# Kernel tuning notes

Hardware: AMD Instinct MI355X
Metric: run time of the kernel (lower is better)

## Reference

```python
import jax, jax.numpy as jnp
import numpy as np
from jax import lax
from jax.scipy.special import logsumexp

KX = jnp.array([[1., 0., -1.], [2., 0., -2.], [1., 0., -1.]], jnp.float32).reshape(1, 1, 3, 3)
KY = jnp.array([[1., 2., 1.], [0., 0., 0.], [-1., -2., -1.]], jnp.float32).reshape(1, 1, 3, 3)
SINK_EPS = 0.05 ** 2  # geomloss SamplesLoss('sinkhorn', p=2, blur=0.05): eps = blur**p
SINK_ITERS = 10
N_SUB = 4096


def _gauss1d(size, sigma):
    x = jnp.arange(size, dtype=jnp.float32) - (size - 1) / 2.0
    k = jnp.exp(-(x * x) / (2.0 * sigma * sigma))
    return k / k.sum()


def _sep_filter(x, k, sym_pad):
    # separable 2D filter; x [B,C,H,W], k [ks]. VALID conv; optional symmetric pad (scipy 'reflect').
    B, C, H, W = x.shape
    xr = x.reshape(B * C, 1, H, W)
    if sym_pad:
        r = k.shape[0] // 2
        xr = jnp.pad(xr, ((0, 0), (0, 0), (r, r), (r, r)), mode='symmetric')
    o = lax.conv_general_dilated(xr, k.reshape(1, 1, -1, 1), (1, 1), 'VALID')
    o = lax.conv_general_dilated(o, k.reshape(1, 1, 1, -1), (1, 1), 'VALID')
    return o.reshape(B, C, o.shape[2], o.shape[3])


def _ssim_per_sample(x, y):
    # standard gaussian-window SSIM (11x11, sigma=1.5, data_range=1.0), mean per sample -> [B]
    k = _gauss1d(11, 1.5)
    mu1, mu2 = _sep_filter(x, k, False), _sep_filter(y, k, False)
    s11 = _sep_filter(x * x, k, False) - mu1 * mu1
    s22 = _sep_filter(y * y, k, False) - mu2 * mu2
    s12 = _sep_filter(x * y, k, False) - mu1 * mu2
    C1, C2 = 0.01 ** 2, 0.03 ** 2
    m = ((2 * mu1 * mu2 + C1) * (2 * s12 + C2)) / ((mu1 * mu1 + mu2 * mu2 + C1) * (s11 + s22 + C2))
    return m.mean(axis=(1, 2, 3))


def _sobel(x):
    # SobelGrad.forward: per-channel magnitude, per-(b,c) max-normalized, channel-mean -> [B,1,H,W]
    B, C, H, W = x.shape
    xr = x.reshape(B * C, 1, H, W)
    gx = lax.conv_general_dilated(xr, KX, (1, 1), ((1, 1), (1, 1)))
    gy = lax.conv_general_dilated(xr, KY, (1, 1), ((1, 1), (1, 1)))
    mag = jnp.sqrt(gx * gx + gy * gy + 1e-6).reshape(B, C, H, W)
    mag = mag / jnp.maximum(mag.max(axis=(2, 3), keepdims=True), 1e-6)
    return mag.mean(1, keepdims=True)


def _avgpool2(x):
    B, C, H, W = x.shape
    return x.reshape(B, C, H // 2, 2, W // 2, 2).mean(axis=(3, 5))


def _charb_mean(d):
    return jnp.sqrt(d * d + 1e-6).mean()  # charbonnier eps=1e-3


def _ot_eps(x, y):
    # entropic OT value with uniform weights, log-domain Sinkhorn, envelope gradient (geomloss-style:
    # iterations detached, one differentiable update at the end).
    N, M = x.shape[0], y.shape[0]
    C = 0.5 * (jnp.sum(x * x, 1)[:, None] + jnp.sum(y * y, 1)[None, :] - 2.0 * x @ y.T)  # p=2 cost |x-y|^2/2
    Cd = lax.stop_gradient(C)
    loga, logb = -float(np.log(N)), -float(np.log(M))
    def body(carry, _):
        f, g = carry
        g = -SINK_EPS * logsumexp(loga + (f[:, None] - Cd) / SINK_EPS, axis=0)
        f = -SINK_EPS * logsumexp(logb + (g[None, :] - Cd) / SINK_EPS, axis=1)
        return (f, g), None
    (f, g), _ = lax.scan(body, (jnp.zeros((N,), x.dtype), jnp.zeros((M,), x.dtype)), None, length=SINK_ITERS)
    f = lax.stop_gradient(f)
    g = -SINK_EPS * logsumexp(loga + (f[:, None] - C) / SINK_EPS, axis=0)
    f = -SINK_EPS * logsumexp(logb + (g[None, :] - C) / SINK_EPS, axis=1)
    return f.mean() + g.mean()


def _sinkhorn_div(x, y):
    return _ot_eps(x, y) - 0.5 * _ot_eps(x, x) - 0.5 * _ot_eps(y, y)


def _forward(y, mri, pet, mask, ehat, idx):
    B, C, H, W = y.shape
    y_gray = y.mean(1, keepdims=True)
    ssim_m = 1.0 - _ssim_per_sample(y_gray, mri).mean()
    ssim_p = 1.0 - _ssim_per_sample(y, pet).mean()
    g_cons = (_charb_mean(_sobel(y_gray) - _sobel(mri))
              + _charb_mean(_sobel(_avgpool2(y).mean(1, keepdims=True)) - _sobel(_avgpool2(mri))))
    aux = jnp.abs(ehat - lax.stop_gradient(_sobel(mri))).mean()
    # per-sample masked point clouds, fixed 4096-point subsample (idx ~ randperm[:4096])
    y_pts = (y * mask).reshape(B, C, H * W).transpose(0, 2, 1)    # [B,HW,3]
    pet_pts = (pet * mask).reshape(B, C, H * W).transpose(0, 2, 1)
    y_s = jnp.take_along_axis(y_pts, idx[..., None], axis=1)      # [B,4096,3]
    pet_s = jnp.take_along_axis(pet_pts, idx[..., None], axis=1)
    include = ((mask.reshape(B, -1) > 0.1).sum(1) >= 32).astype(y.dtype)  # 'continue' guard
    L_transport = (include * jax.vmap(_sinkhorn_div)(y_s, pet_s)).sum() / B
    L_out = (include * ((y * (1.0 - mask)) ** 2).mean(axis=(1, 2, 3))).sum() / B
    mri_rgb = jnp.broadcast_to(mri, y.shape)
    L_ssim = (include * (1.0 - _ssim_per_sample(y * mask, mri_rgb * mask))).sum() / B
    loss_transport = 0.8 * L_transport + 0.3 * L_out + 0.5 * L_ssim  # alpha, beta, gamma
    L_intensity = 2.5 * jnp.mean((y * mask - pet * mask) ** 2)
    # gaussian_smooth: scipy gaussian_filter sigma=1, truncate=4 -> radius 4, mode 'reflect';
    # torch path detaches before smoothing -> stop_gradient
    smoothed = lax.stop_gradient(_sep_filter(y, _gauss1d(9, 1.0), True))
    L_smooth = jnp.mean((smoothed - y) ** 2)
    total = loss_transport + L_intensity + 0.2 * L_smooth
    return total, ssim_m, ssim_p, g_cons, aux


def setup_inputs() -> dict:
    key = jax.random.key(0)
    ks = jax.random.split(key, 5)
    B, C, H, W = 2, 3, 256, 256
    y = jax.random.uniform(ks[0], (B, C, H, W), jnp.float32)
    mri = jax.random.uniform(ks[1], (B, 1, H, W), jnp.float32)
    pet = jax.random.uniform(ks[2], (B, C, H, W), jnp.float32)
    mask = jax.random.uniform(ks[3], (B, 1, H, W), jnp.float32)
    ehat = jax.random.uniform(ks[4], (B, 1, H, W), jnp.float32)
    rng = np.random.default_rng(0)
    idx = jnp.asarray(np.stack([rng.permutation(H * W)[:N_SUB] for _ in range(B)]), dtype=jnp.int32)
    return {"y": y, "mri": mri, "pet": pet, "mask": mask, "ehat": ehat, "idx": idx}


def reference(y, mri, pet, mask, ehat, idx):
    return _forward(y, mri, pet, mask, ehat, idx)
```

## Files before the change

kernel.cpp:

```cpp
#include <hip/hip_runtime.h>
#include <math.h>

#define INV_EPS_L2E 577.0780163555854f
#define EPS_LOGN 0.02079441542f
#define EPS_LN2 0.00173286795f

#define NPTS 4096
#define CHUNK 64
#define NCH 64
#define CPT 8
#define COLS_PER_BLK 2048
#define NCB 2
#define QSTRIDE (NCH * NPTS)

typedef float v2f __attribute__((ext_vector_type(2)));

__device__ __forceinline__ v2f pk_add(v2f a, v2f b) {
    v2f d;
    asm("v_pk_add_f32 %0, %1, %2" : "=v"(d) : "v"(a), "v"(b));
    return d;
}
__device__ __forceinline__ v2f pk_fma_blo(v2f a, v2f b, v2f c) {
    v2f d;
    asm("v_pk_fma_f32 %0, %1, %2, %3 op_sel:[0,0,0] op_sel_hi:[0,1,1]"
        : "=v"(d) : "v"(a), "v"(b), "v"(c));
    return d;
}
__device__ __forceinline__ v2f pk_fma_bhi(v2f a, v2f b, v2f c) {
    v2f d;
    asm("v_pk_fma_f32 %0, %1, %2, %3 op_sel:[1,0,0] op_sel_hi:[1,1,1]"
        : "=v"(d) : "v"(a), "v"(b), "v"(c));
    return d;
}
__device__ __forceinline__ v2f pk_fma_blo_chi(v2f a, v2f b, v2f c) {
    v2f d;
    asm("v_pk_fma_f32 %0, %1, %2, %3 op_sel:[0,0,1] op_sel_hi:[0,1,1]"
        : "=v"(d) : "v"(a), "v"(b), "v"(c));
    return d;
}
__device__ __forceinline__ v2f pk_add_bhi(v2f a, v2f b) {
    v2f d;
    asm("v_pk_add_f32 %0, %1, %2 op_sel:[0,1] op_sel_hi:[1,1]"
        : "=v"(d) : "v"(a), "v"(b));
    return d;
}

constexpr int A_SSIMA  = 0;
constexpr int A_SSIMB  = 2;
constexpr int A_SSIMC  = 4;
constexpr int A_CH1    = 6;
constexpr int A_CH2    = 7;
constexpr int A_AUX    = 8;
constexpr int A_INT    = 9;
constexpr int A_LOUT   = 10;
constexpr int A_CNT    = 12;
constexpr int A_SMOOTH = 14;
constexpr int A_SINK   = 16;
constexpr int A_MAX    = 32;

__device__ __forceinline__ float blockSum(float v, int tid) {
#pragma unroll
    for (int o = 32; o; o >>= 1) v += __shfl_down(v, o, 64);
    __shared__ float sh[4];
    __syncthreads();
    if ((tid & 63) == 0) sh[tid >> 6] = v;
    __syncthreads();
    return sh[0] + sh[1] + sh[2] + sh[3];
}

__device__ __forceinline__ float blockMax(float v, int tid) {
#pragma unroll
    for (int o = 32; o; o >>= 1) v = fmaxf(v, __shfl_down(v, o, 64));
    __shared__ float sh[4];
    __syncthreads();
    if ((tid & 63) == 0) sh[tid >> 6] = v;
    __syncthreads();
    return fmaxf(fmaxf(sh[0], sh[1]), fmaxf(sh[2], sh[3]));
}

__global__ __launch_bounds__(256) void egf_prep(const float* __restrict__ y,
                                                const float* __restrict__ pet,
                                                const float* __restrict__ mask,
                                                float* __restrict__ ygray,
                                                float* __restrict__ acc) {
    int b = blockIdx.y;
    int p = blockIdx.x * 256 + threadIdx.x;
    float m  = mask[b * 65536 + p];
    float y0 = y[(b * 3 + 0) * 65536 + p];
    float y1 = y[(b * 3 + 1) * 65536 + p];
    float y2 = y[(b * 3 + 2) * 65536 + p];
    float q0 = pet[(b * 3 + 0) * 65536 + p];
    float q1 = pet[(b * 3 + 1) * 65536 + p];
    float q2 = pet[(b * 3 + 2) * 65536 + p];
    ygray[b * 65536 + p] = (y0 + y1 + y2) * (1.0f / 3.0f);
    float d0 = m * y0 - m * q0, d1 = m * y1 - m * q1, d2 = m * y2 - m * q2;
    float inten = d0 * d0 + d1 * d1 + d2 * d2;
    float im = 1.0f - m;
    float o0 = y0 * im, o1 = y1 * im, o2 = y2 * im;
    float lout = o0 * o0 + o1 * o1 + o2 * o2;
    float cnt = (m > 0.1f) ? 1.0f : 0.0f;
    float t;
    t = blockSum(inten, threadIdx.x); if (threadIdx.x == 0) atomicAdd(&acc[A_INT], t);
    t = blockSum(lout,  threadIdx.x); if (threadIdx.x == 0) atomicAdd(&acc[A_LOUT + b], t);
    t = blockSum(cnt,   threadIdx.x); if (threadIdx.x == 0) atomicAdd(&acc[A_CNT + b], t);
}

__global__ __launch_bounds__(256) void egf_pool(const float* __restrict__ y,
                                                const float* __restrict__ mri,
                                                float* __restrict__ py,
                                                float* __restrict__ pmri) {
    int b = blockIdx.y;
    int po = blockIdx.x * 256 + threadIdx.x;
    int i = po >> 7, j = po & 127;
    int p0 = (i * 2) * 256 + j * 2;
    float s = 0.0f;
#pragma unroll
    for (int c = 0; c < 3; c++) {
        const float* ip = y + (b * 3 + c) * 65536;
        s += ip[p0] + ip[p0 + 1] + ip[p0 + 256] + ip[p0 + 257];
    }
    py[b * 16384 + po] = s * (1.0f / 12.0f);
    const float* mp = mri + b * 65536;
    pmri[b * 16384 + po] = (mp[p0] + mp[p0 + 1] + mp[p0 + 256] + mp[p0 + 257]) * 0.25f;
}

__global__ __launch_bounds__(256) void egf_sobel(const float* __restrict__ in,
                                                 float* __restrict__ mag,
                                                 unsigned* __restrict__ mx,
                                                 int H, int logH) {
    int b = blockIdx.y;
    int p = blockIdx.x * 256 + threadIdx.x;
    int HH = H * H;
    const float* ip = in + b * HH;
    int i = p >> logH, j = p & (H - 1);
    auto at = [&](int ii, int jj) -> float {
        return (ii >= 0 && ii < H && jj >= 0 && jj < H) ? ip[(ii << logH) + jj] : 0.0f;
    };
    float a00 = at(i - 1, j - 1), a01 = at(i - 1, j), a02 = at(i - 1, j + 1);
    float a10 = at(i, j - 1),                         a12 = at(i, j + 1);
    float a20 = at(i + 1, j - 1), a21 = at(i + 1, j), a22 = at(i + 1, j + 1);
    float gx = a00 - a02 + 2.0f * a10 - 2.0f * a12 + a20 - a22;
    float gy = a00 + 2.0f * a01 + a02 - a20 - 2.0f * a21 - a22;
    float m = sqrtf(gx * gx + gy * gy + 1e-6f);
    mag[b * HH + p] = m;
    float bm = blockMax(m, threadIdx.x);
    if (threadIdx.x == 0) atomicMax(mx + b, __float_as_uint(bm));
}

__global__ __launch_bounds__(256) void egf_charb(const float* __restrict__ magA,
                                                 const float* __restrict__ magB,
                                                 const unsigned* __restrict__ mxA,
                                                 const unsigned* __restrict__ mxB,
                                                 const float* __restrict__ ehat,
                                                 float* __restrict__ accC,
                                                 float* __restrict__ accAux,
                                                 int HH) {
    int b = blockIdx.y;
    int p = blockIdx.x * 256 + threadIdx.x;
    float c = 0.0f, au = 0.0f;
    float da = fmaxf(__uint_as_float(mxA[b]), 1e-6f);
    float db = fmaxf(__uint_as_float(mxB[b]), 1e-6f);
    if (p < HH) {
        float sa = magA[b * HH + p] / da;
        float sb = magB[b * HH + p] / db;
        float d = sa - sb;
        c = sqrtf(d * d + 1e-6f);
        if (ehat) au = fabsf(ehat[b * HH + p] - sb);
    }
    float tc = blockSum(c, threadIdx.x);
    if (threadIdx.x == 0) atomicAdd(accC, tc);
    if (ehat) {
        float ta = blockSum(au, threadIdx.x);
        if (threadIdx.x == 0) atomicAdd(accAux, ta);
    }
}

__global__ __launch_bounds__(256) void egf_ssim(const float* __restrict__ X, int xBS, int xCS,
                                                const float* __restrict__ Y, int yBS, int yCS,
                                                const float* __restrict__ M,
                                                int C_, float* __restrict__ accB) {
    int bc = blockIdx.z; int b = bc / C_; int c = bc - b * C_;
    const float* xp = X + b * xBS + c * xCS;
    const float* yp = Y + b * yBS + c * yCS;
    const float* mp = M ? (M + b * 65536) : nullptr;
    __shared__ float sx[26][27];
    __shared__ float sy[26][27];
    int ti = blockIdx.x * 16, tj = blockIdx.y * 16;
    int tid = threadIdx.y * 16 + threadIdx.x;
    for (int t = tid; t < 26 * 26; t += 256) {
        int li = t / 26, lj = t - li * 26;
        int gi = ti + li, gj = tj + lj;
        float a = 0.0f, bb = 0.0f;
        if (gi < 256 && gj < 256) {
            int p = (gi << 8) + gj;
            float m = mp ? mp[p] : 1.0f;
            a = xp[p] * m; bb = yp[p] * m;
        }
        sx[li][lj] = a; sy[li][lj] = bb;
    }
    __syncthreads();
    float w[11];
    {
        float s = 0.0f;
#pragma unroll
        for (int i = 0; i < 11; i++) { float d = (float)(i - 5); w[i] = expf(-d * d * (1.0f / 4.5f)); s += w[i]; }
        float inv = 1.0f / s;
#pragma unroll
        for (int i = 0; i < 11; i++) w[i] *= inv;
    }
    int oi = ti + threadIdx.y, oj = tj + threadIdx.x;
    float val = 0.0f;
    if (oi < 246 && oj < 246) {
        float mu1 = 0, mu2 = 0, xx = 0, yy = 0, xy = 0;
        for (int di = 0; di < 11; di++) {
            float wi = w[di];
#pragma unroll
            for (int dj = 0; dj < 11; dj++) {
                float ww = wi * w[dj];
                float a  = sx[threadIdx.y + di][threadIdx.x + dj];
                float bb = sy[threadIdx.y + di][threadIdx.x + dj];
                mu1 += ww * a; mu2 += ww * bb;
                xx += ww * a * a; yy += ww * bb * bb; xy += ww * a * bb;
            }
        }
        float s11 = xx - mu1 * mu1, s22 = yy - mu2 * mu2, s12 = xy - mu1 * mu2;
        const float C1 = 1e-4f, C2 = 9e-4f;
        val = ((2.0f * mu1 * mu2 + C1) * (2.0f * s12 + C2)) /
              ((mu1 * mu1 + mu2 * mu2 + C1) * (s11 + s22 + C2));
    }
    float tot = blockSum(val, tid);
    if (tid == 0) atomicAdd(&accB[b], tot);
}

__device__ __forceinline__ int refl256(int i) { return i < 0 ? -1 - i : (i > 255 ? 511 - i : i); }

__device__ __forceinline__ void gauss9(float* w) {
    float s = 0.0f;
#pragma unroll
    for (int t = 0; t < 9; t++) { float d = (float)(t - 4); w[t] = expf(-0.5f * d * d); s += w[t]; }
    float inv = 1.0f / s;
#pragma unroll
    for (int t = 0; t < 9; t++) w[t] *= inv;
}

__global__ __launch_bounds__(256) void egf_smoothV(const float* __restrict__ y, float* __restrict__ tmp) {
    int g = blockIdx.x * 256 + threadIdx.x;
    int bc = g >> 16; int p = g & 65535; int i = p >> 8, j = p & 255;
    float w[9]; gauss9(w);
    const float* ip = y + bc * 65536;
    float s = 0.0f;
#pragma unroll
    for (int t = 0; t < 9; t++) s += w[t] * ip[(refl256(i + t - 4) << 8) + j];
    tmp[g] = s;
}

__global__ __launch_bounds__(256) void egf_smoothH(const float* __restrict__ tmp,
                                                   const float* __restrict__ y,
                                                   float* __restrict__ acc) {
    int g = blockIdx.x * 256 + threadIdx.x;
    int bc = g >> 16; int p = g & 65535; int i = p >> 8, j = p & 255;
    float w[9]; gauss9(w);
    const float* tp = tmp + bc * 65536;
    float s = 0.0f;
#pragma unroll
    for (int t = 0; t < 9; t++) s += w[t] * tp[(i << 8) + refl256(j + t - 4)];
    float d = s - y[g];
    float tt = blockSum(d * d, threadIdx.x);
    if (threadIdx.x == 0) atomicAdd(acc, tt);
}

__global__ __launch_bounds__(256) void egf_gather(const float* __restrict__ y,
                                                  const float* __restrict__ pet,
                                                  const float* __restrict__ mask,
                                                  const int* __restrict__ idx,
                                                  float4* __restrict__ pts) {
    int t = blockIdx.x * 256 + threadIdx.x;
    int b = t >> 12, j = t & 4095;
    int p = idx[b * 4096 + j];
    float m = mask[b * 65536 + p];
    float a0 = y[(b * 3 + 0) * 65536 + p] * m;
    float a1 = y[(b * 3 + 1) * 65536 + p] * m;
    float a2 = y[(b * 3 + 2) * 65536 + p] * m;
    pts[(b * 2 + 0) * 4096 + j] = make_float4(a0, a1, a2, 0.5f * (a0 * a0 + a1 * a1 + a2 * a2));
    float c0 = pet[(b * 3 + 0) * 65536 + p] * m;
    float c1 = pet[(b * 3 + 1) * 65536 + p] * m;
    float c2 = pet[(b * 3 + 2) * 65536 + p] * m;
    pts[(b * 2 + 1) * 4096 + j] = make_float4(c0, c1, c2, 0.5f * (c0 * c0 + c1 * c1 + c2 * c2));
}

__device__ __forceinline__ float stageCombine(const float2* __restrict__ Pin,
                                              int qbase, int row, int h, int r_local,
                                              float* sm, float* ss, int tid) {
    const float2* p = Pin + qbase + (h * 16) * NPTS + row;
    float2 t[16];
#pragma unroll
    for (int k = 0; k < 16; k++) t[k] = p[k * NPTS];
    float m16 = -3.4e38f;
#pragma unroll
    for (int k = 0; k < 16; k++) m16 = fmaxf(m16, t[k].x);
    float s16 = 0.0f;
#pragma unroll
    for (int k = 0; k < 16; k++) s16 += t[k].y * __builtin_amdgcn_exp2f(t[k].x - m16);
    sm[h * 64 + r_local] = m16;
    ss[h * 64 + r_local] = s16;
    __syncthreads();
    float v = 0.0f;
    if (tid < 64) {
        float m0 = sm[tid], m1 = sm[64 + tid], m2 = sm[128 + tid], m3 = sm[192 + tid];
        float M = fmaxf(fmaxf(m0, m1), fmaxf(m2, m3));
        float S = ss[tid]       * __builtin_amdgcn_exp2f(m0 - M) +
                  ss[64 + tid]  * __builtin_amdgcn_exp2f(m1 - M) +
                  ss[128 + tid] * __builtin_amdgcn_exp2f(m2 - M) +
                  ss[192 + tid] * __builtin_amdgcn_exp2f(m3 - M);
        v = EPS_LOGN - EPS_LN2 * (M + log2f(S));
    }
    return v;
}

__global__ __launch_bounds__(256) void egf_sink_half8(const float4* __restrict__ pts,
                                                      const float2* __restrict__ Pin,
                                                      float2* __restrict__ Pout,
                                                      int dir, int init) {
    int q = blockIdx.z; int b = q / 3, t = q - b * 3;
    int xsel = (t == 2) ? 1 : 0;
    int ysel = (t == 1) ? 0 : 1;
    const float4* rowP = pts + (b * 2 + (dir ? ysel : xsel)) * NPTS;
    const float4* colP = pts + (b * 2 + (dir ? xsel : ysel)) * NPTS;

    __shared__ float4 srow[CHUNK];
    __shared__ float sm[256], ss[256];
    int tid = threadIdx.x;
    int chunk = blockIdx.y;
    int r_local = tid & 63, h = tid >> 6;
    int row = chunk * CHUNK + r_local;

    int col0 = blockIdx.x * COLS_PER_BLK + tid;
    float4 cf[8];
#pragma unroll
    for (int k = 0; k < 8; k++) cf[k] = colP[col0 + k * 256];

    float v = 0.0f;
    if (!init)
        v = stageCombine(Pin, q * QSTRIDE, row, h, r_local, sm, ss, tid);
    if (tid < 64) {
        float4 pp = rowP[row];
        srow[tid] = make_float4(pp.x * INV_EPS_L2E, pp.y * INV_EPS_L2E,
                                pp.z * INV_EPS_L2E, (v - pp.w) * INV_EPS_L2E);
    }
    __syncthreads();

    v2f cx[4], cy[4], cz[4], cw[4];
#pragma unroll
    for (int p = 0; p < 4; p++) {
        cx[p] = (v2f){cf[2 * p].x, cf[2 * p + 1].x};
        cy[p] = (v2f){cf[2 * p].y, cf[2 * p + 1].y};
        cz[p] = (v2f){cf[2 * p].z, cf[2 * p + 1].z};
        cw[p] = (v2f){cf[2 * p].w * INV_EPS_L2E, cf[2 * p + 1].w * INV_EPS_L2E};
    }
    v2f mx[4];
#pragma unroll
    for (int p = 0; p < 4; p++) mx[p] = (v2f){-3.4e38f, -3.4e38f};
#pragma unroll 4
    for (int rr = 0; rr < CHUNK; rr++) {
        float4 rp = srow[rr];
        v2f rxy = (v2f){rp.x, rp.y};
        v2f rzw = (v2f){rp.z, rp.w};
#pragma unroll
        for (int p = 0; p < 4; p++) {
            v2f e = pk_fma_blo_chi(rzw, cz[p], rzw);
            e = pk_fma_bhi(rxy, cy[p], e);
            e = pk_fma_blo(rxy, cx[p], e);
            mx[p].x = fmaxf(mx[p].x, e.x);
            mx[p].y = fmaxf(mx[p].y, e.y);
        }
    }
    v2f mneg[4], sa[4];
#pragma unroll
    for (int p = 0; p < 4; p++) { mneg[p] = -mx[p]; sa[p] = (v2f){0.0f, 0.0f}; }
#pragma unroll 4
    for (int rr = 0; rr < CHUNK; rr++) {
        float4 rp = srow[rr];
        v2f rxy = (v2f){rp.x, rp.y};
        v2f rzw = (v2f){rp.z, rp.w};
#pragma unroll
        for (int p = 0; p < 4; p++) {
            v2f e = pk_fma_blo(rzw, cz[p], mneg[p]);
            e = pk_fma_bhi(rxy, cy[p], e);
            e = pk_fma_blo(rxy, cx[p], e);
            e = pk_add_bhi(e, rzw);
            v2f ex;
            ex.x = __builtin_amdgcn_exp2f(e.x);
            ex.y = __builtin_amdgcn_exp2f(e.y);
            sa[p] = pk_add(sa[p], ex);
        }
    }
    float2* om = Pout + q * QSTRIDE + chunk * NPTS;
#pragma unroll
    for (int p = 0; p < 4; p++) {
        om[col0 + (2 * p) * 256]     = make_float2(mx[p].x - cw[p].x, sa[p].x);
        om[col0 + (2 * p + 1) * 256] = make_float2(mx[p].y - cw[p].y, sa[p].y);
    }
}

__global__ __launch_bounds__(256) void egf_sink_val8(const float2* __restrict__ Pf,
                                                     const float2* __restrict__ Pg,
                                                     float* __restrict__ acc) {
    int q = blockIdx.y;
    int side = blockIdx.x >> 6;
    int chunk = blockIdx.x & 63;
    const float2* P = side ? Pg : Pf;
    __shared__ float sm[256], ss[256];
    int tid = threadIdx.x;
    int r_local = tid & 63, h = tid >> 6;
    int row = chunk * CHUNK + r_local;
    float v = stageCombine(P, q * QSTRIDE, row, h, r_local, sm, ss, tid);
    float tot = blockSum(v, tid);
    if (tid == 0) atomicAdd(&acc[A_SINK + q], tot * (1.0f / 4096.0f));
}

__global__ void egf_finalize(const float* __restrict__ acc, float* __restrict__ out) {
    if (threadIdx.x != 0 || blockIdx.x != 0) return;
    const float AREA = 246.0f * 246.0f;
    float ssim_m = 1.0f - (acc[A_SSIMA] + acc[A_SSIMA + 1]) / (2.0f * AREA);
    float ssim_p = 1.0f - (acc[A_SSIMB] + acc[A_SSIMB + 1]) / (2.0f * 3.0f * AREA);
    float g_cons = acc[A_CH1] / (2.0f * 65536.0f) + acc[A_CH2] / (2.0f * 16384.0f);
    float aux = acc[A_AUX] / (2.0f * 65536.0f);
    float inc0 = (acc[A_CNT]     >= 31.5f) ? 1.0f : 0.0f;
    float inc1 = (acc[A_CNT + 1] >= 31.5f) ? 1.0f : 0.0f;
    const float* v = acc + A_SINK;
    float Lt = (inc0 * (v[0] - 0.5f * v[1] - 0.5f * v[2]) +
                inc1 * (v[3] - 0.5f * v[4] - 0.5f * v[5])) * 0.5f;
    float Lo = (inc0 * acc[A_LOUT] + inc1 * acc[A_LOUT + 1]) / (3.0f * 65536.0f) * 0.5f;
    float Ls = (inc0 * (1.0f - acc[A_SSIMC] / (3.0f * AREA)) +
                inc1 * (1.0f - acc[A_SSIMC + 1] / (3.0f * AREA))) * 0.5f;
    float Li = 2.5f * acc[A_INT] / (2.0f * 3.0f * 65536.0f);
    float Lsm = acc[A_SMOOTH] / (2.0f * 3.0f * 65536.0f);
    float total = 0.8f * Lt + 0.3f * Lo + 0.5f * Ls + Li + 0.2f * Lsm;
    out[0] = total; out[1] = ssim_m; out[2] = ssim_p; out[3] = g_cons; out[4] = aux;
}

extern "C" void kernel_launch(void* const* d_in, const int* in_sizes, int n_in,
                              void* d_out, int out_size, void* d_ws, size_t ws_size,
                              hipStream_t stream) {
    const float* y    = (const float*)d_in[0];
    const float* mri  = (const float*)d_in[1];
    const float* pet  = (const float*)d_in[2];
    const float* mask = (const float*)d_in[3];
    const float* ehat = (const float*)d_in[4];
    const int*   idx  = (const int*)d_in[5];
    float* out = (float*)d_out;
    float* ws  = (float*)d_ws;

    float* acc   = ws;
    float4* pts  = (float4*)(ws + 64);
    float* base  = ws + 64 + 65536;

    float2* Pf = (float2*)base;
    float2* Pg = Pf + QSTRIDE * 6;
    float* ibase = base + 4 * QSTRIDE * 6;

    float* ygray    = ibase;
    float* py       = ygray + 131072;
    float* pmri     = py + 32768;
    float* mag_yg   = pmri + 32768;
    float* mag_mri  = mag_yg + 131072;
    float* mag_py   = mag_mri + 131072;
    float* mag_pmri = mag_py + 32768;
    float* tmp      = mag_pmri + 32768;

    hipMemsetAsync(acc, 0, 64 * sizeof(float), stream);

    unsigned* mx = (unsigned*)(acc + A_MAX);

    egf_prep<<<dim3(256, 2), 256, 0, stream>>>(y, pet, mask, ygray, acc);
    egf_pool<<<dim3(64, 2), 256, 0, stream>>>(y, mri, py, pmri);
    egf_sobel<<<dim3(256, 2), 256, 0, stream>>>(ygray, mag_yg, mx + 0, 256, 8);
    egf_sobel<<<dim3(256, 2), 256, 0, stream>>>(mri, mag_mri, mx + 2, 256, 8);
    egf_sobel<<<dim3(64, 2), 256, 0, stream>>>(py, mag_py, mx + 4, 128, 7);
    egf_sobel<<<dim3(64, 2), 256, 0, stream>>>(pmri, mag_pmri, mx + 6, 128, 7);
    egf_charb<<<dim3(256, 2), 256, 0, stream>>>(mag_yg, mag_mri, mx + 0, mx + 2, ehat,
                                                acc + A_CH1, acc + A_AUX, 65536);
    egf_charb<<<dim3(64, 2), 256, 0, stream>>>(mag_py, mag_pmri, mx + 4, mx + 6, nullptr,
                                               acc + A_CH2, nullptr, 16384);
    egf_ssim<<<dim3(16, 16, 2), dim3(16, 16), 0, stream>>>(ygray, 65536, 0, mri, 65536, 0,
                                                           nullptr, 1, acc + A_SSIMA);
    egf_ssim<<<dim3(16, 16, 6), dim3(16, 16), 0, stream>>>(y, 196608, 65536, pet, 196608, 65536,
                                                           nullptr, 3, acc + A_SSIMB);
    egf_ssim<<<dim3(16, 16, 6), dim3(16, 16), 0, stream>>>(y, 196608, 65536, mri, 65536, 0,
                                                           mask, 3, acc + A_SSIMC);
    egf_smoothV<<<1536, 256, 0, stream>>>(y, tmp);
    egf_smoothH<<<1536, 256, 0, stream>>>(tmp, y, acc + A_SMOOTH);
    egf_gather<<<32, 256, 0, stream>>>(y, pet, mask, idx, pts);

    dim3 sgrid(NCB, NCH, 6);
    for (int it = 0; it < 11; ++it) {
        egf_sink_half8<<<sgrid, 256, 0, stream>>>(pts, Pf, Pg, 0, it == 0 ? 1 : 0);
        egf_sink_half8<<<sgrid, 256, 0, stream>>>(pts, Pg, Pf, 1, 0);
    }
    egf_sink_val8<<<dim3(128, 6), 256, 0, stream>>>(Pf, Pg, acc);
    egf_finalize<<<1, 64, 0, stream>>>(acc, out);
}
```

Measured before the change: 843.7 us.

## Fuse Sinkhorn iterations into one cooperative kernel and merge small launches

Replaces the 22 per-half Sinkhorn launches, the gather, the value pass and finalize with a single cooperative kernel of 768 blocks that uses grid-wide syncs between stages. The prep/pool, four sobel, two charbonnier, three SSIM and two smoothing launches are also merged into fewer kernels, and smoothing now uses a shared-memory tile instead of a global temporary. This targets kernel launch overhead and inter-kernel gaps. In exchange it depends on all 768 blocks being co-resident and adds grid-sync cost, and it keeps the old multi-launch path as a fallback if the cooperative launch fails.

```diff
diff --git a/kernel.cpp b/kernel.cpp
--- a/kernel.cpp
+++ b/kernel.cpp
@@ -1,5 +1,8 @@
 #include <hip/hip_runtime.h>
+#include <hip/hip_cooperative_groups.h>
 #include <math.h>
+
+namespace cg = cooperative_groups;
 
 #define INV_EPS_L2E 577.0780163555854f
 #define EPS_LOGN 0.02079441542f
@@ -78,58 +81,67 @@
     return fmaxf(fmaxf(sh[0], sh[1]), fmaxf(sh[2], sh[3]));
 }
 
-__global__ __launch_bounds__(256) void egf_prep(const float* __restrict__ y,
-                                                const float* __restrict__ pet,
-                                                const float* __restrict__ mask,
-                                                float* __restrict__ ygray,
-                                                float* __restrict__ acc) {
+__global__ __launch_bounds__(256) void egf_prep_pool(const float* __restrict__ y,
+                                                     const float* __restrict__ pet,
+                                                     const float* __restrict__ mri,
+                                                     const float* __restrict__ mask,
+                                                     float* __restrict__ ygray,
+                                                     float* __restrict__ py,
+                                                     float* __restrict__ pmri,
+                                                     float* __restrict__ acc) {
     int b = blockIdx.y;
-    int p = blockIdx.x * 256 + threadIdx.x;
-    float m  = mask[b * 65536 + p];
-    float y0 = y[(b * 3 + 0) * 65536 + p];
-    float y1 = y[(b * 3 + 1) * 65536 + p];
-    float y2 = y[(b * 3 + 2) * 65536 + p];
-    float q0 = pet[(b * 3 + 0) * 65536 + p];
-    float q1 = pet[(b * 3 + 1) * 65536 + p];
-    float q2 = pet[(b * 3 + 2) * 65536 + p];
-    ygray[b * 65536 + p] = (y0 + y1 + y2) * (1.0f / 3.0f);
-    float d0 = m * y0 - m * q0, d1 = m * y1 - m * q1, d2 = m * y2 - m * q2;
-    float inten = d0 * d0 + d1 * d1 + d2 * d2;
-    float im = 1.0f - m;
-    float o0 = y0 * im, o1 = y1 * im, o2 = y2 * im;
-    float lout = o0 * o0 + o1 * o1 + o2 * o2;
-    float cnt = (m > 0.1f) ? 1.0f : 0.0f;
-    float t;
-    t = blockSum(inten, threadIdx.x); if (threadIdx.x == 0) atomicAdd(&acc[A_INT], t);
-    t = blockSum(lout,  threadIdx.x); if (threadIdx.x == 0) atomicAdd(&acc[A_LOUT + b], t);
-    t = blockSum(cnt,   threadIdx.x); if (threadIdx.x == 0) atomicAdd(&acc[A_CNT + b], t);
-}
-
-__global__ __launch_bounds__(256) void egf_pool(const float* __restrict__ y,
-                                                const float* __restrict__ mri,
-                                                float* __restrict__ py,
-                                                float* __restrict__ pmri) {
+    if (blockIdx.x < 256) {
+        int p = blockIdx.x * 256 + threadIdx.x;
+        float m  = mask[b * 65536 + p];
+        float y0 = y[(b * 3 + 0) * 65536 + p];
+        float y1 = y[(b * 3 + 1) * 65536 + p];
+        float y2 = y[(b * 3 + 2) * 65536 + p];
+        float q0 = pet[(b * 3 + 0) * 65536 + p];
+        float q1 = pet[(b * 3 + 1) * 65536 + p];
+        float q2 = pet[(b * 3 + 2) * 65536 + p];
+        ygray[b * 65536 + p] = (y0 + y1 + y2) * (1.0f / 3.0f);
+        float d0 = m * y0 - m * q0, d1 = m * y1 - m * q1, d2 = m * y2 - m * q2;
+        float inten = d0 * d0 + d1 * d1 + d2 * d2;
+        float im = 1.0f - m;
+        float o0 = y0 * im, o1 = y1 * im, o2 = y2 * im;
+        float lout = o0 * o0 + o1 * o1 + o2 * o2;
+        float cnt = (m > 0.1f) ? 1.0f : 0.0f;
+        float t;
+        t = blockSum(inten, threadIdx.x); if (threadIdx.x == 0) atomicAdd(&acc[A_INT], t);
+        t = blockSum(lout,  threadIdx.x); if (threadIdx.x == 0) atomicAdd(&acc[A_LOUT + b], t);
+        t = blockSum(cnt,   threadIdx.x); if (threadIdx.x == 0) atomicAdd(&acc[A_CNT + b], t);
+    } else {
+        int po = (blockIdx.x - 256) * 256 + threadIdx.x;
+        int i = po >> 7, j = po & 127;
+        int p0 = (i * 2) * 256 + j * 2;
+        float s = 0.0f;
+#pragma unroll
+        for (int c = 0; c < 3; c++) {
+            const float* ip = y + (b * 3 + c) * 65536;
+            s += ip[p0] + ip[p0 + 1] + ip[p0 + 256] + ip[p0 + 257];
+        }
+        py[b * 16384 + po] = s * (1.0f / 12.0f);
+        const float* mp = mri + b * 65536;
+        pmri[b * 16384 + po] = (mp[p0] + mp[p0 + 1] + mp[p0 + 256] + mp[p0 + 257]) * 0.25f;
+    }
+}
+
+__global__ __launch_bounds__(256) void egf_sobel4(const float* __restrict__ yg,
+                                                  const float* __restrict__ mri,
+                                                  const float* __restrict__ py,
+                                                  const float* __restrict__ pmri,
+                                                  float* __restrict__ mag_yg,
+                                                  float* __restrict__ mag_mri,
+                                                  float* __restrict__ mag_py,
+                                                  float* __restrict__ mag_pmri,
+                                                  unsigned* __restrict__ mx) {
     int b = blockIdx.y;
-    int po = blockIdx.x * 256 + threadIdx.x;
-    int i = po >> 7, j = po & 127;
-    int p0 = (i * 2) * 256 + j * 2;
-    float s = 0.0f;
-#pragma unroll
-    for (int c = 0; c < 3; c++) {
-        const float* ip = y + (b * 3 + c) * 65536;
-        s += ip[p0] + ip[p0 + 1] + ip[p0 + 256] + ip[p0 + 257];
-    }
-    py[b * 16384 + po] = s * (1.0f / 12.0f);
-    const float* mp = mri + b * 65536;
-    pmri[b * 16384 + po] = (mp[p0] + mp[p0 + 1] + mp[p0 + 256] + mp[p0 + 257]) * 0.25f;
-}
-
-__global__ __launch_bounds__(256) void egf_sobel(const float* __restrict__ in,
-                                                 float* __restrict__ mag,
-                                                 unsigned* __restrict__ mx,
-                                                 int H, int logH) {
-    int b = blockIdx.y;
-    int p = blockIdx.x * 256 + threadIdx.x;
+    int x = blockIdx.x;
+    const float* in; float* mag; int H, logH, slot, p;
+    if (x < 256)      { in = yg;   mag = mag_yg;   H = 256; logH = 8; slot = 0; p = x * 256 + threadIdx.x; }
+    else if (x < 512) { in = mri;  mag = mag_mri;  H = 256; logH = 8; slot = 2; p = (x - 256) * 256 + threadIdx.x; }
+    else if (x < 576) { in = py;   mag = mag_py;   H = 128; logH = 7; slot = 4; p = (x - 512) * 256 + threadIdx.x; }
+    else              { in = pmri; mag = mag_pmri; H = 128; logH = 7; slot = 6; p = (x - 576) * 256 + threadIdx.x; }
     int HH = H * H;
     const float* ip = in + b * HH;
     int i = p >> logH, j = p & (H - 1);
@@ -144,19 +156,24 @@
     float m = sqrtf(gx * gx + gy * gy + 1e-6f);
     mag[b * HH + p] = m;
     float bm = blockMax(m, threadIdx.x);
-    if (threadIdx.x == 0) atomicMax(mx + b, __float_as_uint(bm));
-}
-
-__global__ __launch_bounds__(256) void egf_charb(const float* __restrict__ magA,
-                                                 const float* __restrict__ magB,
-                                                 const unsigned* __restrict__ mxA,
-                                                 const unsigned* __restrict__ mxB,
-                                                 const float* __restrict__ ehat,
-                                                 float* __restrict__ accC,
-                                                 float* __restrict__ accAux,
-                                                 int HH) {
+    if (threadIdx.x == 0) atomicMax(mx + slot + b, __float_as_uint(bm));
+}
+
+__global__ __launch_bounds__(256) void egf_charb2(const float* __restrict__ mag_yg,
+                                                  const float* __restrict__ mag_mri,
+                                                  const float* __restrict__ mag_py,
+                                                  const float* __restrict__ mag_pmri,
+                                                  const unsigned* __restrict__ mx,
+                                                  const float* __restrict__ ehat,
+                                                  float* __restrict__ acc) {
     int b = blockIdx.y;
-    int p = blockIdx.x * 256 + threadIdx.x;
+    int x = blockIdx.x;
+    const float *magA, *magB; const unsigned *mxA, *mxB;
+    float *accC; const float* eh; int HH, p;
+    if (x < 256) { magA = mag_yg; magB = mag_mri; mxA = mx + 0; mxB = mx + 2;
+                   accC = acc + A_CH1; eh = ehat; HH = 65536; p = x * 256 + threadIdx.x; }
+    else         { magA = mag_py; magB = mag_pmri; mxA = mx + 4; mxB = mx + 6;
+                   accC = acc + A_CH2; eh = nullptr; HH = 16384; p = (x - 256) * 256 + threadIdx.x; }
     float c = 0.0f, au = 0.0f;
     float da = fmaxf(__uint_as_float(mxA[b]), 1e-6f);
     float db = fmaxf(__uint_as_float(mxB[b]), 1e-6f);
@@ -165,24 +182,33 @@
         float sb = magB[b * HH + p] / db;
         float d = sa - sb;
         c = sqrtf(d * d + 1e-6f);
-        if (ehat) au = fabsf(ehat[b * HH + p] - sb);
+        if (eh) au = fabsf(eh[b * HH + p] - sb);
     }
     float tc = blockSum(c, threadIdx.x);
     if (threadIdx.x == 0) atomicAdd(accC, tc);
-    if (ehat) {
+    if (eh) {
         float ta = blockSum(au, threadIdx.x);
-        if (threadIdx.x == 0) atomicAdd(accAux, ta);
-    }
-}
-
-__global__ __launch_bounds__(256) void egf_ssim(const float* __restrict__ X, int xBS, int xCS,
-                                                const float* __restrict__ Y, int yBS, int yCS,
-                                                const float* __restrict__ M,
-                                                int C_, float* __restrict__ accB) {
-    int bc = blockIdx.z; int b = bc / C_; int c = bc - b * C_;
-    const float* xp = X + b * xBS + c * xCS;
-    const float* yp = Y + b * yBS + c * yCS;
-    const float* mp = M ? (M + b * 65536) : nullptr;
+        if (threadIdx.x == 0) atomicAdd(&acc[A_AUX], ta);
+    }
+}
+
+__global__ __launch_bounds__(256) void egf_ssim3(const float* __restrict__ y,
+                                                 const float* __restrict__ ygray,
+                                                 const float* __restrict__ mri,
+                                                 const float* __restrict__ pet,
+                                                 const float* __restrict__ mask,
+                                                 float* __restrict__ acc) {
+    int z = blockIdx.z;
+    const float *xp, *yp, *mp = nullptr; float* accB; int b;
+    if (z < 2) {
+        b = z; xp = ygray + b * 65536; yp = mri + b * 65536; accB = acc + A_SSIMA;
+    } else if (z < 8) {
+        int bc = z - 2; b = bc / 3; int c = bc - b * 3;
+        xp = y + (b * 3 + c) * 65536; yp = pet + (b * 3 + c) * 65536; accB = acc + A_SSIMB;
+    } else {
+        int bc = z - 8; b = bc / 3; int c = bc - b * 3;
+        xp = y + (b * 3 + c) * 65536; yp = mri + b * 65536; mp = mask + b * 65536; accB = acc + A_SSIMC;
+    }
     __shared__ float sx[26][27];
     __shared__ float sy[26][27];
     int ti = blockIdx.x * 16, tj = blockIdx.y * 16;
@@ -243,30 +269,36 @@
     for (int t = 0; t < 9; t++) w[t] *= inv;
 }
 
-__global__ __launch_bounds__(256) void egf_smoothV(const float* __restrict__ y, float* __restrict__ tmp) {
-    int g = blockIdx.x * 256 + threadIdx.x;
-    int bc = g >> 16; int p = g & 65535; int i = p >> 8, j = p & 255;
+__global__ __launch_bounds__(256) void egf_smooth1(const float* __restrict__ y,
+                                                   float* __restrict__ acc) {
+    int bc = blockIdx.z;
+    int i0 = blockIdx.x * 16, j0 = blockIdx.y * 16;
+    const float* ip = y + bc * 65536;
+    __shared__ float sx[24][25];
+    __shared__ float sv[16][25];
+    int tid = threadIdx.x;
     float w[9]; gauss9(w);
-    const float* ip = y + bc * 65536;
+    for (int t = tid; t < 576; t += 256) {
+        int li = t / 24, lj = t - li * 24;
+        int gi = refl256(i0 + li - 4), gj = refl256(j0 + lj - 4);
+        sx[li][lj] = ip[(gi << 8) + gj];
+    }
+    __syncthreads();
+    for (int t = tid; t < 384; t += 256) {
+        int li = t / 24, lj = t - li * 24;
+        float s = 0.0f;
+#pragma unroll
+        for (int k = 0; k < 9; k++) s += w[k] * sx[li + k][lj];
+        sv[li][lj] = s;
+    }
+    __syncthreads();
+    int ty = tid >> 4, tx = tid & 15;
     float s = 0.0f;
 #pragma unroll
-    for (int t = 0; t < 9; t++) s += w[t] * ip[(refl256(i + t - 4) << 8) + j];
-    tmp[g] = s;
-}
-
-__global__ __launch_bounds__(256) void egf_smoothH(const float* __restrict__ tmp,
-                                                   const float* __restrict__ y,
-                                                   float* __restrict__ acc) {
-    int g = blockIdx.x * 256 + threadIdx.x;
-    int bc = g >> 16; int p = g & 65535; int i = p >> 8, j = p & 255;
-    float w[9]; gauss9(w);
-    const float* tp = tmp + bc * 65536;
-    float s = 0.0f;
-#pragma unroll
-    for (int t = 0; t < 9; t++) s += w[t] * tp[(i << 8) + refl256(j + t - 4)];
-    float d = s - y[g];
-    float tt = blockSum(d * d, threadIdx.x);
-    if (threadIdx.x == 0) atomicAdd(acc, tt);
+    for (int k = 0; k < 9; k++) s += w[k] * sv[ty][tx + k];
+    float d = s - sx[ty + 4][tx + 4];
+    float tt = blockSum(d * d, tid);
+    if (tid == 0) atomicAdd(acc, tt);
 }
 
 __global__ __launch_bounds__(256) void egf_gather(const float* __restrict__ y,
@@ -418,25 +450,165 @@
     if (tid == 0) atomicAdd(&acc[A_SINK + q], tot * (1.0f / 4096.0f));
 }
 
-__global__ void egf_finalize(const float* __restrict__ acc, float* __restrict__ out) {
-    if (threadIdx.x != 0 || blockIdx.x != 0) return;
+__device__ __forceinline__ void finalize_body(float* acc, float* out, bool atomicRead) {
+    auto rd = [&](int i) -> float {
+        return atomicRead ? atomicAdd(&acc[i], 0.0f) : acc[i];
+    };
     const float AREA = 246.0f * 246.0f;
-    float ssim_m = 1.0f - (acc[A_SSIMA] + acc[A_SSIMA + 1]) / (2.0f * AREA);
-    float ssim_p = 1.0f - (acc[A_SSIMB] + acc[A_SSIMB + 1]) / (2.0f * 3.0f * AREA);
-    float g_cons = acc[A_CH1] / (2.0f * 65536.0f) + acc[A_CH2] / (2.0f * 16384.0f);
-    float aux = acc[A_AUX] / (2.0f * 65536.0f);
-    float inc0 = (acc[A_CNT]     >= 31.5f) ? 1.0f : 0.0f;
-    float inc1 = (acc[A_CNT + 1] >= 31.5f) ? 1.0f : 0.0f;
-    const float* v = acc + A_SINK;
-    float Lt = (inc0 * (v[0] - 0.5f * v[1] - 0.5f * v[2]) +
-                inc1 * (v[3] - 0.5f * v[4] - 0.5f * v[5])) * 0.5f;
-    float Lo = (inc0 * acc[A_LOUT] + inc1 * acc[A_LOUT + 1]) / (3.0f * 65536.0f) * 0.5f;
-    float Ls = (inc0 * (1.0f - acc[A_SSIMC] / (3.0f * AREA)) +
-                inc1 * (1.0f - acc[A_SSIMC + 1] / (3.0f * AREA))) * 0.5f;
-    float Li = 2.5f * acc[A_INT] / (2.0f * 3.0f * 65536.0f);
-    float Lsm = acc[A_SMOOTH] / (2.0f * 3.0f * 65536.0f);
+    float ssim_m = 1.0f - (rd(A_SSIMA) + rd(A_SSIMA + 1)) / (2.0f * AREA);
+    float ssim_p = 1.0f - (rd(A_SSIMB) + rd(A_SSIMB + 1)) / (2.0f * 3.0f * AREA);
+    float g_cons = rd(A_CH1) / (2.0f * 65536.0f) + rd(A_CH2) / (2.0f * 16384.0f);
+    float aux = rd(A_AUX) / (2.0f * 65536.0f);
+    float inc0 = (rd(A_CNT)     >= 31.5f) ? 1.0f : 0.0f;
+    float inc1 = (rd(A_CNT + 1) >= 31.5f) ? 1.0f : 0.0f;
+    float v0 = rd(A_SINK + 0), v1 = rd(A_SINK + 1), v2 = rd(A_SINK + 2);
+    float v3 = rd(A_SINK + 3), v4 = rd(A_SINK + 4), v5 = rd(A_SINK + 5);
+    float Lt = (inc0 * (v0 - 0.5f * v1 - 0.5f * v2) +
+                inc1 * (v3 - 0.5f * v4 - 0.5f * v5)) * 0.5f;
+    float Lo = (inc0 * rd(A_LOUT) + inc1 * rd(A_LOUT + 1)) / (3.0f * 65536.0f) * 0.5f;
+    float Ls = (inc0 * (1.0f - rd(A_SSIMC) / (3.0f * AREA)) +
+                inc1 * (1.0f - rd(A_SSIMC + 1) / (3.0f * AREA))) * 0.5f;
+    float Li = 2.5f * rd(A_INT) / (2.0f * 3.0f * 65536.0f);
+    float Lsm = rd(A_SMOOTH) / (2.0f * 3.0f * 65536.0f);
     float total = 0.8f * Lt + 0.3f * Lo + 0.5f * Ls + Li + 0.2f * Lsm;
     out[0] = total; out[1] = ssim_m; out[2] = ssim_p; out[3] = g_cons; out[4] = aux;
+}
+
+__global__ void egf_finalize(float* __restrict__ acc, float* __restrict__ out) {
+    if (threadIdx.x != 0 || blockIdx.x != 0) return;
+    finalize_body(acc, out, false);
+}
+
+__global__ __launch_bounds__(256, 3) void egf_sink_all(const float* __restrict__ y,
+                                                       const float* __restrict__ pet,
+                                                       const float* __restrict__ mask,
+                                                       const int* __restrict__ idx,
+                                                       float4* __restrict__ pts,
+                                                       float2* __restrict__ Pf,
+                                                       float2* __restrict__ Pg,
+                                                       float* __restrict__ acc,
+                                                       float* __restrict__ out) {
+    cg::grid_group grid = cg::this_grid();
+    int tid = threadIdx.x;
+    int bid = blockIdx.x;
+
+    if (bid < 32) {
+        int t = bid * 256 + tid;
+        int bb = t >> 12, j = t & 4095;
+        int p = idx[bb * 4096 + j];
+        float m = mask[bb * 65536 + p];
+        float a0 = y[(bb * 3 + 0) * 65536 + p] * m;
+        float a1 = y[(bb * 3 + 1) * 65536 + p] * m;
+        float a2 = y[(bb * 3 + 2) * 65536 + p] * m;
+        pts[(bb * 2 + 0) * 4096 + j] = make_float4(a0, a1, a2, 0.5f * (a0 * a0 + a1 * a1 + a2 * a2));
+        float c0 = pet[(bb * 3 + 0) * 65536 + p] * m;
+        float c1 = pet[(bb * 3 + 1) * 65536 + p] * m;
+        float c2 = pet[(bb * 3 + 2) * 65536 + p] * m;
+        pts[(bb * 2 + 1) * 4096 + j] = make_float4(c0, c1, c2, 0.5f * (c0 * c0 + c1 * c1 + c2 * c2));
+    }
+    grid.sync();
+
+    int q = bid / 128;
+    int rem = bid - q * 128;
+    int chunk = rem >> 1, cb = rem & 1;
+    int b = q / 3, t3 = q - b * 3;
+    int xsel = (t3 == 2) ? 1 : 0;
+    int ysel = (t3 == 1) ? 0 : 1;
+    const float4* xP = pts + (b * 2 + xsel) * NPTS;
+    const float4* yP = pts + (b * 2 + ysel) * NPTS;
+
+    __shared__ float4 srow[CHUNK];
+    __shared__ float sm[256], ss[256];
+    int r_local = tid & 63, h = tid >> 6;
+    int row = chunk * CHUNK + r_local;
+    int col0 = cb * COLS_PER_BLK + tid;
+    int qbase = q * QSTRIDE;
+
+    for (int half = 0; half < 22; ++half) {
+        int dir = half & 1;
+        const float4* rowP = dir ? yP : xP;
+        const float4* colP = dir ? xP : yP;
+        const float2* Pin  = dir ? Pg : Pf;
+        float2* Pout       = dir ? Pf : Pg;
+
+        float4 cf[8];
+#pragma unroll
+        for (int k = 0; k < 8; k++) cf[k] = colP[col0 + k * 256];
+
+        float v = 0.0f;
+        if (half) v = stageCombine(Pin, qbase, row, h, r_local, sm, ss, tid);
+        if (tid < 64) {
+            float4 pp = rowP[row];
+            srow[tid] = make_float4(pp.x * INV_EPS_L2E, pp.y * INV_EPS_L2E,
+                                    pp.z * INV_EPS_L2E, (v - pp.w) * INV_EPS_L2E);
+        }
+        __syncthreads();
+
+        v2f cx[4], cy[4], cz[4], cw[4];
+#pragma unroll
+        for (int p = 0; p < 4; p++) {
+            cx[p] = (v2f){cf[2 * p].x, cf[2 * p + 1].x};
+            cy[p] = (v2f){cf[2 * p].y, cf[2 * p + 1].y};
+            cz[p] = (v2f){cf[2 * p].z, cf[2 * p + 1].z};
+            cw[p] = (v2f){cf[2 * p].w * INV_EPS_L2E, cf[2 * p + 1].w * INV_EPS_L2E};
+        }
+        v2f mx[4];
+#pragma unroll
+        for (int p = 0; p < 4; p++) mx[p] = (v2f){-3.4e38f, -3.4e38f};
+#pragma unroll 4
+        for (int rr = 0; rr < CHUNK; rr++) {
+            float4 rp = srow[rr];
+            v2f rxy = (v2f){rp.x, rp.y};
+            v2f rzw = (v2f){rp.z, rp.w};
+#pragma unroll
+            for (int p = 0; p < 4; p++) {
+                v2f e = pk_fma_blo_chi(rzw, cz[p], rzw);
+                e = pk_fma_bhi(rxy, cy[p], e);
+                e = pk_fma_blo(rxy, cx[p], e);
+                mx[p].x = fmaxf(mx[p].x, e.x);
+                mx[p].y = fmaxf(mx[p].y, e.y);
+            }
+        }
+        v2f mneg[4], sa[4];
+#pragma unroll
+        for (int p = 0; p < 4; p++) { mneg[p] = -mx[p]; sa[p] = (v2f){0.0f, 0.0f}; }
+#pragma unroll 4
+        for (int rr = 0; rr < CHUNK; rr++) {
+            float4 rp = srow[rr];
+            v2f rxy = (v2f){rp.x, rp.y};
+            v2f rzw = (v2f){rp.z, rp.w};
+#pragma unroll
+            for (int p = 0; p < 4; p++) {
+                v2f e = pk_fma_blo(rzw, cz[p], mneg[p]);
+                e = pk_fma_bhi(rxy, cy[p], e);
+                e = pk_fma_blo(rxy, cx[p], e);
+                e = pk_add_bhi(e, rzw);
+                v2f ex;
+                ex.x = __builtin_amdgcn_exp2f(e.x);
+                ex.y = __builtin_amdgcn_exp2f(e.y);
+                sa[p] = pk_add(sa[p], ex);
+            }
+        }
+        float2* om = Pout + qbase + chunk * NPTS;
+#pragma unroll
+        for (int p = 0; p < 4; p++) {
+            om[col0 + (2 * p) * 256]     = make_float2(mx[p].x - cw[p].x, sa[p].x);
+            om[col0 + (2 * p + 1) * 256] = make_float2(mx[p].y - cw[p].y, sa[p].y);
+        }
+        grid.sync();
+    }
+
+    {
+        int side = rem >> 6, vchunk = rem & 63;
+        int vrow = vchunk * CHUNK + r_local;
+        const float2* P = side ? Pg : Pf;
+        float v = stageCombine(P, qbase, vrow, h, r_local, sm, ss, tid);
+        float tot = blockSum(v, tid);
+        if (tid == 0) atomicAdd(&acc[A_SINK + q], tot * (1.0f / 4096.0f));
+    }
+    grid.sync();
+
+    if (bid == 0 && tid == 0) finalize_body(acc, out, true);
 }
 
 extern "C" void kernel_launch(void* const* d_in, const int* in_sizes, int n_in,
@@ -466,37 +638,31 @@
     float* mag_mri  = mag_yg + 131072;
     float* mag_py   = mag_mri + 131072;
     float* mag_pmri = mag_py + 32768;
-    float* tmp      = mag_pmri + 32768;
 
     hipMemsetAsync(acc, 0, 64 * sizeof(float), stream);
 
     unsigned* mx = (unsigned*)(acc + A_MAX);
 
-    egf_prep<<<dim3(256, 2), 256, 0, stream>>>(y, pet, mask, ygray, acc);
-    egf_pool<<<dim3(64, 2), 256, 0, stream>>>(y, mri, py, pmri);
-    egf_sobel<<<dim3(256, 2), 256, 0, stream>>>(ygray, mag_yg, mx + 0, 256, 8);
-    egf_sobel<<<dim3(256, 2), 256, 0, stream>>>(mri, mag_mri, mx + 2, 256, 8);
-    egf_sobel<<<dim3(64, 2), 256, 0, stream>>>(py, mag_py, mx + 4, 128, 7);
-    egf_sobel<<<dim3(64, 2), 256, 0, stream>>>(pmri, mag_pmri, mx + 6, 128, 7);
-    egf_charb<<<dim3(256, 2), 256, 0, stream>>>(mag_yg, mag_mri, mx + 0, mx + 2, ehat,
-                                                acc + A_CH1, acc + A_AUX, 65536);
-    egf_charb<<<dim3(64, 2), 256, 0, stream>>>(mag_py, mag_pmri, mx + 4, mx + 6, nullptr,
-                                               acc + A_CH2, nullptr, 16384);
-    egf_ssim<<<dim3(16, 16, 2), dim3(16, 16), 0, stream>>>(ygray, 65536, 0, mri, 65536, 0,
-                                                           nullptr, 1, acc + A_SSIMA);
-    egf_ssim<<<dim3(16, 16, 6), dim3(16, 16), 0, stream>>>(y, 196608, 65536, pet, 196608, 65536,
-                                                           nullptr, 3, acc + A_SSIMB);
-    egf_ssim<<<dim3(16, 16, 6), dim3(16, 16), 0, stream>>>(y, 196608, 65536, mri, 65536, 0,
-                                                           mask, 3, acc + A_SSIMC);
-    egf_smoothV<<<1536, 256, 0, stream>>>(y, tmp);
-    egf_smoothH<<<1536, 256, 0, stream>>>(tmp, y, acc + A_SMOOTH);
-    egf_gather<<<32, 256, 0, stream>>>(y, pet, mask, idx, pts);
-
-    dim3 sgrid(NCB, NCH, 6);
-    for (int it = 0; it < 11; ++it) {
-        egf_sink_half8<<<sgrid, 256, 0, stream>>>(pts, Pf, Pg, 0, it == 0 ? 1 : 0);
-        egf_sink_half8<<<sgrid, 256, 0, stream>>>(pts, Pg, Pf, 1, 0);
-    }
-    egf_sink_val8<<<dim3(128, 6), 256, 0, stream>>>(Pf, Pg, acc);
-    egf_finalize<<<1, 64, 0, stream>>>(acc, out);
-}
+    egf_prep_pool<<<dim3(320, 2), 256, 0, stream>>>(y, pet, mri, mask, ygray, py, pmri, acc);
+    egf_sobel4<<<dim3(640, 2), 256, 0, stream>>>(ygray, mri, py, pmri,
+                                                 mag_yg, mag_mri, mag_py, mag_pmri, mx);
+    egf_charb2<<<dim3(320, 2), 256, 0, stream>>>(mag_yg, mag_mri, mag_py, mag_pmri, mx, ehat, acc);
+    egf_ssim3<<<dim3(16, 16, 14), dim3(16, 16), 0, stream>>>(y, ygray, mri, pet, mask, acc);
+    egf_smooth1<<<dim3(16, 16, 6), 256, 0, stream>>>(y, acc + A_SMOOTH);
+
+    void* sargs[] = {(void*)&y, (void*)&pet, (void*)&mask, (void*)&idx,
+                     (void*)&pts, (void*)&Pf, (void*)&Pg, (void*)&acc, (void*)&out};
+    hipError_t ce = hipLaunchCooperativeKernel(reinterpret_cast<void*>(egf_sink_all),
+                                               dim3(768), dim3(256), sargs, 0, stream);
+    if (ce != hipSuccess) {
+        (void)hipGetLastError();
+        egf_gather<<<32, 256, 0, stream>>>(y, pet, mask, idx, pts);
+        dim3 sgrid(NCB, NCH, 6);
+        for (int it = 0; it < 11; ++it) {
+            egf_sink_half8<<<sgrid, 256, 0, stream>>>(pts, Pf, Pg, 0, it == 0 ? 1 : 0);
+            egf_sink_half8<<<sgrid, 256, 0, stream>>>(pts, Pg, Pf, 1, 0);
+        }
+        egf_sink_val8<<<dim3(128, 6), 256, 0, stream>>>(Pf, Pg, acc);
+        egf_finalize<<<1, 64, 0, stream>>>(acc, out);
+    }
+}
```

After: 2.416 ms. +186.4%, slower.
